# Kernel tuning notes

Measured on AMD Instinct MI355X. Metric: run time of the kernel, lower is better.

## Reference

```python
import jax, jax.numpy as jnp
import numpy as np

B, N, IN_DIM, EMB, HEADS, M, ITERS = 8, 4096, 1024, 512, 4, 256, 6
DH = EMB // HEADS
SCALE = DH ** -0.5
RES_K = 33  # residual depthwise conv kernel size (TransMIL / nystrom-attention default)


def setup_inputs() -> dict:
    key = jax.random.key(0)
    ks = iter(jax.random.split(key, 40))
    def rn(shape, s=0.02):
        return jax.random.normal(next(ks), shape, jnp.float32) * s
    inp = {"X": jax.random.normal(next(ks), (B, N, IN_DIM), jnp.float32)}
    inp["few_w"] = rn((IN_DIM, EMB)); inp["few_b"] = jnp.zeros((EMB,), jnp.float32)
    inp["cls_token"] = rn((1, 1, EMB), 1.0)
    for i in (1, 2):
        inp[f"l{i}_ln_g"] = jnp.ones((EMB,), jnp.float32)
        inp[f"l{i}_ln_b"] = jnp.zeros((EMB,), jnp.float32)
        inp[f"l{i}_qkv_w"] = rn((EMB, 3 * EMB))
        inp[f"l{i}_out_w"] = rn((EMB, EMB))
        inp[f"l{i}_out_b"] = jnp.zeros((EMB,), jnp.float32)
        inp[f"l{i}_res_k"] = rn((HEADS, 1, RES_K, 1))
    for ksz in (7, 5, 3):
        inp[f"ppeg_k{ksz}"] = rn((EMB, 1, ksz, ksz))
        inp[f"ppeg_b{ksz}"] = jnp.zeros((EMB,), jnp.float32)
    inp["norm_g"] = jnp.ones((EMB,), jnp.float32)
    inp["norm_b"] = jnp.zeros((EMB,), jnp.float32)
    inp["cls_w"] = rn((EMB, 1)); inp["cls_b"] = jnp.zeros((1,), jnp.float32)
    return inp


def _ln(x, g, b):
    mu = x.mean(-1, keepdims=True)
    var = x.var(-1, keepdims=True)
    return (x - mu) / jnp.sqrt(var + 1e-5) * g + b


def _pinv(x, iters):
    # Moore-Penrose iterative pseudo-inverse of (..., m, m)
    abs_x = jnp.abs(x)
    z = jnp.swapaxes(x, -1, -2) / (abs_x.sum(-1).max() * abs_x.sum(-2).max())
    I = jnp.eye(x.shape[-1], dtype=x.dtype)
    for _ in range(iters):
        xz = x @ z
        z = 0.25 * z @ (13 * I - xz @ (15 * I - xz @ (7 * I - xz)))
    return z


def _nystrom_layer(x, ln_g, ln_b, qkv_w, out_w, out_b, res_k):
    # pre-norm transformer layer with Nystrom attention + residual depthwise conv
    b, n, d = x.shape
    h = _ln(x, ln_g, ln_b)
    pad = (-n) % M  # left-pad so seq divisible by n_landmarks
    hp = jnp.pad(h, ((0, 0), (pad, 0), (0, 0)))
    n_p = n + pad
    q, k, v = jnp.split(hp @ qkv_w, 3, axis=-1)
    def to_heads(t):
        return t.reshape(b, n_p, HEADS, DH).transpose(0, 2, 1, 3)  # (b,h,n,dh)
    q, k, v = to_heads(q) * SCALE, to_heads(k), to_heads(v)
    l = n_p // M
    q_l = q.reshape(b, HEADS, M, l, DH).mean(3)  # landmark means
    k_l = k.reshape(b, HEADS, M, l, DH).mean(3)
    a1 = jax.nn.softmax(jnp.einsum('bhid,bhjd->bhij', q, k_l), -1)    # (b,h,n,m)
    a2 = jax.nn.softmax(jnp.einsum('bhid,bhjd->bhij', q_l, k_l), -1)  # (b,h,m,m)
    a3 = jax.nn.softmax(jnp.einsum('bhid,bhjd->bhij', q_l, k), -1)    # (b,h,m,n)
    out = a1 @ (_pinv(a2, ITERS) @ (a3 @ v))
    # residual depthwise conv over sequence, one channel per head
    res = jax.lax.conv_general_dilated(
        v, res_k, (1, 1), ((RES_K // 2, RES_K // 2), (0, 0)),
        dimension_numbers=('NCHW', 'OIHW', 'NCHW'), feature_group_count=HEADS)
    out = out + res
    out = out.transpose(0, 2, 1, 3).reshape(b, n_p, d) @ out_w + out_b
    return x + out[:, -n:]


def _dwconv(x, k, bias, pad):
    y = jax.lax.conv_general_dilated(
        x, k, (1, 1), ((pad, pad), (pad, pad)),
        dimension_numbers=('NCHW', 'OIHW', 'NCHW'), feature_group_count=EMB)
    return y + bias[None, :, None, None]


def _ppeg(x, H, W, k7, b7, k5, b5, k3, b3):
    b, _, c = x.shape
    cls_t, feat = x[:, :1], x[:, 1:]
    f = feat.transpose(0, 2, 1).reshape(b, c, H, W)
    y = f + _dwconv(f, k7, b7, 3) + _dwconv(f, k5, b5, 2) + _dwconv(f, k3, b3, 1)
    y = y.reshape(b, c, H * W).transpose(0, 2, 1)
    return jnp.concatenate([cls_t, y], axis=1)


def _forward(X, few_w, few_b, cls_token,
             l1_ln_g, l1_ln_b, l1_qkv_w, l1_out_w, l1_out_b, l1_res_k,
             l2_ln_g, l2_ln_b, l2_qkv_w, l2_out_w, l2_out_b, l2_res_k,
             ppeg_k7, ppeg_b7, ppeg_k5, ppeg_b5, ppeg_k3, ppeg_b3,
             norm_g, norm_b, cls_w, cls_b):
    b, bag = X.shape[0], X.shape[1]
    h = X @ few_w + few_b
    ps = int(np.ceil(np.sqrt(bag)))
    add = ps * ps - bag
    h = jnp.concatenate([h, h[:, :add]], axis=1)  # pad bag to perfect square
    h = jnp.concatenate([jnp.broadcast_to(cls_token, (b, 1, EMB)), h], axis=1)
    h = _nystrom_layer(h, l1_ln_g, l1_ln_b, l1_qkv_w, l1_out_w, l1_out_b, l1_res_k)
    h = _ppeg(h, ps, ps, ppeg_k7, ppeg_b7, ppeg_k5, ppeg_b5, ppeg_k3, ppeg_b3)
    h = _nystrom_layer(h, l2_ln_g, l2_ln_b, l2_qkv_w, l2_out_w, l2_out_b, l2_res_k)
    h = _ln(h, norm_g, norm_b)
    return (h[:, 0] @ cls_w + cls_b).squeeze(-1)  # (batch,) bag logits


def reference(X, few_w, few_b, cls_token,
              l1_ln_g, l1_ln_b, l1_qkv_w, l1_out_w, l1_out_b, l1_res_k,
              l2_ln_g, l2_ln_b, l2_qkv_w, l2_out_w, l2_out_b, l2_res_k,
              ppeg_k7, ppeg_b7, ppeg_k5, ppeg_b5, ppeg_k3, ppeg_b3,
              norm_g, norm_b, cls_w, cls_b):
    return _forward(X, few_w, few_b, cls_token,
                    l1_ln_g, l1_ln_b, l1_qkv_w, l1_out_w, l1_out_b, l1_res_k,
                    l2_ln_g, l2_ln_b, l2_qkv_w, l2_out_w, l2_out_b, l2_res_k,
                    ppeg_k7, ppeg_b7, ppeg_k5, ppeg_b5, ppeg_k3, ppeg_b3,
                    norm_g, norm_b, cls_w, cls_b)
```

## Files before the change

### kernel.cpp

```cpp
#include <hip/hip_runtime.h>

constexpr int BATCH = 8;
constexpr int NTOK  = 4097;
constexpr int NP    = 4352;
constexpr int PADR  = 255;
constexpr int EMBD  = 512;
constexpr int DHD   = 128;
constexpr int LSUB  = 17;
constexpr float SCALE_F = 0.08838834764831845f;

constexpr int PPS   = 72;
constexpr int PPLN  = 72 * 70;
constexpr long long TPAD_FLOATS = (long long)BATCH * EMBD * PPLN;

typedef unsigned short u16;
typedef short   s16x8 __attribute__((ext_vector_type(8)));
typedef u16     u16x4 __attribute__((ext_vector_type(4)));
typedef float   f32x4 __attribute__((ext_vector_type(4)));

__device__ __forceinline__ u16 f2bf(float x) {
    unsigned u = __float_as_uint(x);
    u += 0x7fffu + ((u >> 16) & 1u);
    return (u16)(u >> 16);
}
__device__ __forceinline__ float bf2f(u16 h) {
    return __uint_as_float(((unsigned)h) << 16);
}

__device__ __forceinline__ float block_sum256(float v) {
    __shared__ float tmp[4];
    __syncthreads();
#pragma unroll
    for (int off = 32; off > 0; off >>= 1) v += __shfl_down(v, off, 64);
    int t = threadIdx.x;
    if ((t & 63) == 0) tmp[t >> 6] = v;
    __syncthreads();
    return tmp[0] + tmp[1] + tmp[2] + tmp[3];
}

__device__ __forceinline__ float block_max256(float v) {
    __shared__ float tmp[4];
    __syncthreads();
#pragma unroll
    for (int off = 32; off > 0; off >>= 1) v = fmaxf(v, __shfl_down(v, off, 64));
    int t = threadIdx.x;
    if ((t & 63) == 0) tmp[t >> 6] = v;
    __syncthreads();
    return fmaxf(fmaxf(tmp[0], tmp[1]), fmaxf(tmp[2], tmp[3]));
}

struct GemmP {
    const float* A; const float* B; float* C; const float* bias;
    long long As1, As2, Bs1, Bs2, Cs1, Cs2;
    int Adiv, Bdiv, Cdiv;
    int Am, Bk, Bn, Cm, Arow, Crow;
    int M, N, K, nb;
    float alpha; int accum;
    float bdiagc; int btrans; float cdiagc; int ctrans;
};

constexpr int LDSTR = 40;
constexpr int AH = 0, AL = 2560, BHs = 5120, BLs = 7680;

__global__ __launch_bounds__(256) void gemm_k(GemmP p) {
    __shared__ u16 lds[10240];
    const int bz = blockIdx.z;
    const float* Ab = p.A + (long long)(bz / p.Adiv) * p.As1 + (long long)(bz % p.Adiv) * p.As2;
    const float* Bb = p.B + (long long)(bz / p.Bdiv) * p.Bs1 + (long long)(bz % p.Bdiv) * p.Bs2;
    float*       Cb = p.C + (long long)(bz / p.Cdiv) * p.Cs1 + (long long)(bz % p.Cdiv) * p.Cs2;
    const int m0 = blockIdx.y * 64, n0 = blockIdx.x * 64;
    const int t = threadIdx.x;
    const int wave = t >> 6, lane = t & 63;
    const int wm = (wave & 1) * 32, wn = (wave >> 1) * 32;
    const int quad = lane >> 4, l15 = lane & 15;

    f32x4 acc[2][2];
#pragma unroll
    for (int i = 0; i < 2; ++i)
#pragma unroll
        for (int j = 0; j < 2; ++j) acc[i][j] = (f32x4){0.f, 0.f, 0.f, 0.f};

    for (int k0 = 0; k0 < p.K; k0 += 32) {
        {
            const int ar = t >> 2, ac = (t & 3) * 8;
            float v[8];
            if (m0 + ar < p.M) {
                const float* s = Ab + (long long)(m0 + ar + p.Arow) * p.Am + (k0 + ac);
                float4 x0 = *(const float4*)s, x1 = *(const float4*)(s + 4);
                v[0] = x0.x; v[1] = x0.y; v[2] = x0.z; v[3] = x0.w;
                v[4] = x1.x; v[5] = x1.y; v[6] = x1.z; v[7] = x1.w;
            } else {
#pragma unroll
                for (int i = 0; i < 8; ++i) v[i] = 0.f;
            }
            u16 h[8], l[8];
#pragma unroll
            for (int i = 0; i < 8; ++i) { h[i] = f2bf(v[i]); l[i] = f2bf(v[i] - bf2f(h[i])); }
            const int off = ar * LDSTR + ac;
            u16x4 a0, a1, b0, b1;
#pragma unroll
            for (int i = 0; i < 4; ++i) { a0[i] = h[i]; a1[i] = h[i + 4]; b0[i] = l[i]; b1[i] = l[i + 4]; }
            *(u16x4*)&lds[AH + off] = a0; *(u16x4*)&lds[AH + off + 4] = a1;
            *(u16x4*)&lds[AL + off] = b0; *(u16x4*)&lds[AL + off + 4] = b1;
        }
        if (p.Bn == 1) {
            const int bk = t >> 3, n8 = (t & 7) * 8;
            const float* s = Bb + (long long)(k0 + bk) * p.Bk + (n0 + n8);
            float4 x0 = *(const float4*)s, x1 = *(const float4*)(s + 4);
            float v[8] = {x0.x, x0.y, x0.z, x0.w, x1.x, x1.y, x1.z, x1.w};
            if (p.btrans) {
                const int gk = k0 + bk;
#pragma unroll
                for (int i = 0; i < 8; ++i)
                    v[i] = (gk == n0 + n8 + i ? p.bdiagc : 0.f) - v[i];
            }
#pragma unroll
            for (int i = 0; i < 8; ++i) {
                int j = (i + (t & 7)) & 7;
                u16 h = f2bf(v[j]);
                lds[BHs + (n8 + j) * LDSTR + bk] = h;
                lds[BLs + (n8 + j) * LDSTR + bk] = f2bf(v[j] - bf2f(h));
            }
        } else {
            const int bn = t >> 2, k8 = (t & 3) * 8;
            const float* s = Bb + (long long)(n0 + bn) * p.Bn + (k0 + k8);
            float4 x0 = *(const float4*)s, x1 = *(const float4*)(s + 4);
            float v[8] = {x0.x, x0.y, x0.z, x0.w, x1.x, x1.y, x1.z, x1.w};
            u16 h[8], l[8];
#pragma unroll
            for (int i = 0; i < 8; ++i) { h[i] = f2bf(v[i]); l[i] = f2bf(v[i] - bf2f(h[i])); }
            const int off = bn * LDSTR + k8;
            u16x4 a0, a1, b0, b1;
#pragma unroll
            for (int i = 0; i < 4; ++i) { a0[i] = h[i]; a1[i] = h[i + 4]; b0[i] = l[i]; b1[i] = l[i + 4]; }
            *(u16x4*)&lds[BHs + off] = a0; *(u16x4*)&lds[BHs + off + 4] = a1;
            *(u16x4*)&lds[BLs + off] = b0; *(u16x4*)&lds[BLs + off + 4] = b1;
        }
        __syncthreads();

        s16x8 ah[2], al[2], bh[2], bl[2];
#pragma unroll
        for (int mi = 0; mi < 2; ++mi) {
            const int off = (wm + mi * 16 + l15) * LDSTR + quad * 8;
            u16x4 q0 = *(const u16x4*)&lds[AH + off], q1 = *(const u16x4*)&lds[AH + off + 4];
            u16x4 r0 = *(const u16x4*)&lds[AL + off], r1 = *(const u16x4*)&lds[AL + off + 4];
            s16x8 fh, fl;
#pragma unroll
            for (int i = 0; i < 4; ++i) { fh[i] = q0[i]; fh[i + 4] = q1[i]; fl[i] = r0[i]; fl[i + 4] = r1[i]; }
            ah[mi] = fh; al[mi] = fl;
        }
#pragma unroll
        for (int ni = 0; ni < 2; ++ni) {
            const int off = (wn + ni * 16 + l15) * LDSTR + quad * 8;
            u16x4 q0 = *(const u16x4*)&lds[BHs + off], q1 = *(const u16x4*)&lds[BHs + off + 4];
            u16x4 r0 = *(const u16x4*)&lds[BLs + off], r1 = *(const u16x4*)&lds[BLs + off + 4];
            s16x8 fh, fl;
#pragma unroll
            for (int i = 0; i < 4; ++i) { fh[i] = q0[i]; fh[i + 4] = q1[i]; fl[i] = r0[i]; fl[i + 4] = r1[i]; }
            bh[ni] = fh; bl[ni] = fl;
        }
#pragma unroll
        for (int mi = 0; mi < 2; ++mi)
#pragma unroll
            for (int ni = 0; ni < 2; ++ni) {
                acc[mi][ni] = __builtin_amdgcn_mfma_f32_16x16x32_bf16(ah[mi], bh[ni], acc[mi][ni], 0, 0, 0);
                acc[mi][ni] = __builtin_amdgcn_mfma_f32_16x16x32_bf16(ah[mi], bl[ni], acc[mi][ni], 0, 0, 0);
                acc[mi][ni] = __builtin_amdgcn_mfma_f32_16x16x32_bf16(al[mi], bh[ni], acc[mi][ni], 0, 0, 0);
            }
        __syncthreads();
    }

#pragma unroll
    for (int mi = 0; mi < 2; ++mi)
#pragma unroll
        for (int ni = 0; ni < 2; ++ni) {
            const int n = n0 + wn + ni * 16 + l15;
#pragma unroll
            for (int r = 0; r < 4; ++r) {
                const int m = m0 + wm + mi * 16 + quad * 4 + r;
                if (m >= p.M) continue;
                float v = p.alpha * acc[mi][ni][r];
                if (p.bias) v += p.bias[n];
                if (p.ctrans) v = (m == n ? p.cdiagc : 0.f) - v;
                float* dst = Cb + (long long)(m + p.Crow) * p.Cm + n;
                if (p.accum) *dst += v; else *dst = v;
            }
        }
}

struct SplitP {
    const float* src; u16* dh; u16* dl;
    long long s1, s2, rstride, dstride, total;
    int div, R, C8;
    float scale;
};
__global__ __launch_bounds__(256) void split_k(SplitP p) {
    long long idx = (long long)blockIdx.x * 256 + threadIdx.x;
    if (idx >= p.total) return;
    int c8 = (int)(idx % p.C8);
    long long tmp = idx / p.C8;
    int r  = (int)(tmp % p.R);
    int bz = (int)(tmp / p.R);
    const float* s = p.src + (long long)(bz / p.div) * p.s1 + (long long)(bz % p.div) * p.s2
                   + (long long)r * p.rstride + c8 * 8;
    float4 x0 = *(const float4*)s, x1 = *(const float4*)(s + 4);
    float v[8] = {x0.x, x0.y, x0.z, x0.w, x1.x, x1.y, x1.z, x1.w};
    s16x8 hv, lv;
#pragma unroll
    for (int i = 0; i < 8; ++i) {
        float sv = v[i] * p.scale;
        u16 h = f2bf(sv);
        hv[i] = (short)h;
        lv[i] = (short)f2bf(sv - bf2f(h));
    }
    long long doff = (long long)bz * p.dstride + (long long)r * (p.C8 * 8) + c8 * 8;
    *(s16x8*)&p.dh[doff] = hv;
    *(s16x8*)&p.dl[doff] = lv;
}

__global__ __launch_bounds__(256) void splitT_k(const float* __restrict__ src,
                                                u16* __restrict__ dh, u16* __restrict__ dl,
                                                int K, int N) {
    int idx = blockIdx.x * 256 + threadIdx.x;
    if (idx >= N * K) return;
    int n = idx / K, k = idx - n * K;
    float v = src[(long long)k * N + n];
    u16 h = f2bf(v);
    dh[idx] = h;
    dl[idx] = f2bf(v - bf2f(h));
}

struct GemmBtP {
    const u16 *Ah, *Al, *Bh, *Bl;
    float* C; const float* bias;
    long long Abs, Bbs, Cbs;
    int M, N, K, Cm, Crow, accum;
};

__global__ __launch_bounds__(512, 4) void gemm_bt_k(GemmBtP p) {
    __shared__ u16 lds[10240];
    const int bz = blockIdx.z;
    const u16* Ahb = p.Ah + (long long)bz * p.Abs;
    const u16* Alb = p.Al + (long long)bz * p.Abs;
    const u16* Bhb = p.Bh + (long long)bz * p.Bbs;
    const u16* Blb = p.Bl + (long long)bz * p.Bbs;
    float*     Cb  = p.C  + (long long)bz * p.Cbs;
    const int m0 = blockIdx.y * 128, n0 = blockIdx.x * 256;
    const int t = threadIdx.x;
    const int wave = t >> 6, lane = t & 63;
    const int wm = (wave & 1) * 64, wn = (wave >> 1) * 64;
    const int quad = lane >> 4, l15 = lane & 15;
    const int K = p.K;

    const int r0 = t >> 2, c0 = (t & 3) * 8;
    const int ga0 = (m0 + r0 < p.M) ? (m0 + r0) : (p.M - 1);
    const long long arow0 = (long long)ga0 * K + c0;
    const long long bb0   = (long long)(n0 + wn + l15) * K + quad * 8;
    const long long bstep = 16LL * K;
    const int wof = r0 * LDSTR + c0;

    f32x4 acc[4][4];
#pragma unroll
    for (int i = 0; i < 4; ++i)
#pragma unroll
        for (int j = 0; j < 4; ++j) acc[i][j] = (f32x4){0.f, 0.f, 0.f, 0.f};

    s16x8 sa0, sl0;
    auto LOADA = [&](int k0) {
        sa0 = *(const s16x8*)&Ahb[arow0 + k0];
        sl0 = *(const s16x8*)&Alb[arow0 + k0];
    };
    LOADA(0);

    for (int k0 = 0; k0 < K; k0 += 32) {
        *(s16x8*)&lds[wof]        = sa0;
        *(s16x8*)&lds[5120 + wof] = sl0;
        __syncthreads();
        if (k0 + 32 < K) LOADA(k0 + 32);

        s16x8 bh[4], bl[4];
#pragma unroll
        for (int ni = 0; ni < 4; ++ni) {
            const long long bo = bb0 + ni * bstep + k0;
            bh[ni] = *(const s16x8*)&Bhb[bo];
            bl[ni] = *(const s16x8*)&Blb[bo];
        }
#pragma unroll
        for (int mi = 0; mi < 4; ++mi) {
            const int off = (wm + mi * 16 + l15) * LDSTR + quad * 8;
            s16x8 ah = *(const s16x8*)&lds[off];
            s16x8 al = *(const s16x8*)&lds[5120 + off];
#pragma unroll
            for (int ni = 0; ni < 4; ++ni) {
                acc[mi][ni] = __builtin_amdgcn_mfma_f32_16x16x32_bf16(ah, bh[ni], acc[mi][ni], 0, 0, 0);
                acc[mi][ni] = __builtin_amdgcn_mfma_f32_16x16x32_bf16(ah, bl[ni], acc[mi][ni], 0, 0, 0);
                acc[mi][ni] = __builtin_amdgcn_mfma_f32_16x16x32_bf16(al, bh[ni], acc[mi][ni], 0, 0, 0);
            }
        }
        __syncthreads();
    }

#pragma unroll
    for (int mi = 0; mi < 4; ++mi)
#pragma unroll
        for (int ni = 0; ni < 4; ++ni) {
            const int n = n0 + wn + ni * 16 + l15;
            const float bv = p.bias ? p.bias[n] : 0.f;
#pragma unroll
            for (int r = 0; r < 4; ++r) {
                const int m = m0 + wm + mi * 16 + quad * 4 + r;
                if (m >= p.M) continue;
                float* dst = Cb + (long long)(m + p.Crow) * p.Cm + n;
                float v = acc[mi][ni][r] + bv;
                if (p.accum) *dst += v; else *dst = v;
            }
        }
}

__global__ void cls_set_k(float* H0, const float* cls) {
    int t = blockIdx.x * 256 + threadIdx.x;
    int b = t >> 9, c = t & 511;
    H0[(long long)b * NTOK * EMBD + c] = cls[c];
}

__global__ __launch_bounds__(256) void ln_pad_k(const float* __restrict__ H0,
                                                u16* __restrict__ oh, u16* __restrict__ ol,
                                                const float* g, const float* bb) {
    int row = blockIdx.x, b = blockIdx.y, t = threadIdx.x;
    long long off = ((long long)b * NP + row) * EMBD;
    if (row < PADR) {
        oh[off + t] = 0; oh[off + t + 256] = 0;
        ol[off + t] = 0; ol[off + t + 256] = 0;
        return;
    }
    const float* x = H0 + ((long long)b * NTOK + (row - PADR)) * EMBD;
    float v0 = x[t], v1 = x[t + 256];
    float mu = block_sum256(v0 + v1) * (1.f / EMBD);
    float d0 = v0 - mu, d1 = v1 - mu;
    float var = block_sum256(d0 * d0 + d1 * d1) * (1.f / EMBD);
    float rs = 1.f / sqrtf(var + 1e-5f);
    float y0 = d0 * rs * g[t]       + bb[t];
    float y1 = d1 * rs * g[t + 256] + bb[t + 256];
    u16 h0 = f2bf(y0); oh[off + t]       = h0; ol[off + t]       = f2bf(y0 - bf2f(h0));
    u16 h1 = f2bf(y1); oh[off + t + 256] = h1; ol[off + t + 256] = f2bf(y1 - bf2f(h1));
}

__global__ void landmark_k(const float* __restrict__ QKV, float* __restrict__ QL,
                           float* __restrict__ KL) {
    long long idx = (long long)blockIdx.x * 256 + threadIdx.x;
    int d = idx & 127; int i = (int)((idx >> 7) & 255); int bh = (int)(idx >> 15);
    int b = bh >> 2, h = bh & 3;
    const float* base = QKV + (long long)b * NP * 1536 + (long long)i * LSUB * 1536 + h * DHD + d;
    float sq = 0.f, sk = 0.f;
#pragma unroll
    for (int j = 0; j < LSUB; ++j) { sq += base[j * 1536]; sk += base[j * 1536 + EMBD]; }
    QL[idx] = sq * (1.f / LSUB);
    KL[idx] = sk * (1.f / LSUB);
}

__global__ __launch_bounds__(256) void softmax256_k(float* __restrict__ X) {
    long long row = (long long)blockIdx.x * 4 + (threadIdx.x >> 6);
    int lane = threadIdx.x & 63;
    float4* p = (float4*)(X + row * 256) + lane;
    float4 v = *p;
    float m = fmaxf(fmaxf(v.x, v.y), fmaxf(v.z, v.w));
#pragma unroll
    for (int off = 32; off > 0; off >>= 1) m = fmaxf(m, __shfl_xor(m, off, 64));
    float ex = __expf(v.x - m), ey = __expf(v.y - m), ez = __expf(v.z - m), ew = __expf(v.w - m);
    float s = ex + ey + ez + ew;
#pragma unroll
    for (int off = 32; off > 0; off >>= 1) s += __shfl_xor(s, off, 64);
    float inv = 1.f / s;
    *p = make_float4(ex * inv, ey * inv, ez * inv, ew * inv);
}

__global__ __launch_bounds__(256) void softmax_k(float* __restrict__ X, int L) {
    float4* p = (float4*)(X + (long long)blockIdx.x * L);
    int nv = L >> 2, t = threadIdx.x;
    float m = -1e30f;
    for (int i = t; i < nv; i += 256) {
        float4 v = p[i];
        m = fmaxf(m, fmaxf(fmaxf(v.x, v.y), fmaxf(v.z, v.w)));
    }
    m = block_max256(m);
    float s = 0.f;
    for (int i = t; i < nv; i += 256) {
        float4 v = p[i];
        v.x = __expf(v.x - m); v.y = __expf(v.y - m); v.z = __expf(v.z - m); v.w = __expf(v.w - m);
        p[i] = v;
        s += v.x + v.y + v.z + v.w;
    }
    s = block_sum256(s);
    float inv = 1.f / s;
    for (int i = t; i < nv; i += 256) {
        float4 v = p[i];
        p[i] = make_float4(v.x * inv, v.y * inv, v.z * inv, v.w * inv);
    }
}

__global__ __launch_bounds__(256) void pinv_absmax_k(const float* __restrict__ X, float* red) {
    int bh = blockIdx.x, t = threadIdx.x;
    const float* x = X + (long long)bh * 65536;
    float rs = 0.f, cs = 0.f;
    for (int j = 0; j < 256; ++j) { rs += fabsf(x[t * 256 + j]); cs += fabsf(x[j * 256 + t]); }
    float mr = block_max256(rs);
    float mc = block_max256(cs);
    if (t == 0) { red[bh] = mr; red[32 + bh] = mc; }
}

__global__ void pinv_scalar_k(const float* red, float* inv) {
    float mr = 0.f, mc = 0.f;
    for (int i = 0; i < 32; ++i) { mr = fmaxf(mr, red[i]); mc = fmaxf(mc, red[32 + i]); }
    inv[0] = 1.f / (mr * mc);
}

__global__ void pinv_tinit_k(const float* __restrict__ X, const float* __restrict__ inv,
                             float* __restrict__ Z) {
    long long idx = (long long)blockIdx.x * 256 + threadIdx.x;
    int j = (int)(idx & 255); int i = (int)((idx >> 8) & 255); long long bh = idx >> 16;
    Z[idx] = X[(bh << 16) + ((long long)j << 8) + i] * inv[0];
}

__global__ void resconv_k(const float* __restrict__ QKV, const float* __restrict__ rk,
                          float* __restrict__ ATT2) {
    long long idx = (long long)blockIdx.x * 256 + threadIdx.x;
    if (idx >= (long long)BATCH * NTOK * EMBD) return;
    int c = (int)(idx & 511); long long r = idx >> 9;
    int n = PADR + (int)(r % NTOK); int b = (int)(r / NTOK);
    int h = c >> 7, d = c & 127;
    const float* vb = QKV + (long long)b * NP * 1536 + 1024 + h * DHD + d;
    float acc = 0.f;
#pragma unroll
    for (int u = 0; u < 33; ++u) {
        int nn = n + u - 16;
        if (nn >= 0 && nn < NP) acc += vb[(long long)nn * 1536] * rk[h * 33 + u];
    }
    ATT2[((long long)b * NP + n) * EMBD + c] += acc;
}

__global__ void wsum_k(const float* __restrict__ k7, const float* __restrict__ k5,
                       const float* __restrict__ k3, const float* __restrict__ b7,
                       const float* __restrict__ b5, const float* __restrict__ b3,
                       float* __restrict__ W) {
    int idx = blockIdx.x * 256 + threadIdx.x;
    if (idx < 25088) {
        int c = idx / 49, i = idx - c * 49;
        int dy = i / 7, dx = i - dy * 7;
        float w = k7[idx];
        if (dy >= 1 && dy <= 5 && dx >= 1 && dx <= 5) w += k5[c * 25 + (dy - 1) * 5 + (dx - 1)];
        if (dy >= 2 && dy <= 4 && dx >= 2 && dx <= 4) w += k3[c * 9 + (dy - 2) * 3 + (dx - 2)];
        W[idx] = w;
    } else if (idx < 25600) {
        int c = idx - 25088;
        W[25088 + c] = b7[c] + b5[c] + b3[c];
    }
}

__global__ __launch_bounds__(256) void tin_k(const float* __restrict__ H0,
                                             float* __restrict__ Tpad) {
    __shared__ float lds[64][65];
    const int y = blockIdx.x, c0 = blockIdx.y * 64, b = blockIdx.z;
    const int t = threadIdx.x;
    const int pc = t & 63, pr4 = t >> 6;
    const float* src = H0 + ((long long)b * NTOK + 1 + y * 64) * EMBD + c0;
#pragma unroll
    for (int i = 0; i < 16; ++i) {
        int pr = pr4 + i * 4;
        lds[pr][pc] = src[(long long)pr * EMBD + pc];
    }
    __syncthreads();
    const int xw = t & 63, cw4 = t >> 6;
#pragma unroll
    for (int i = 0; i < 16; ++i) {
        int cw = cw4 + i * 4;
        Tpad[(long long)(b * 512 + c0 + cw) * PPLN + (3 + y) * PPS + 3 + xw] = lds[xw][cw];
    }
}

__global__ __launch_bounds__(256, 4) void conv7_k(const float* __restrict__ Tpad,
                                                  const float* __restrict__ Wall,
                                                  float* __restrict__ Tout) {
    const int bc = blockIdx.x;
    const int c = bc & 511;
    const int t = threadIdx.x;
    const int x = t & 63, band = t >> 6;
    const int y0 = band * 16;
    const float* in = Tpad + (long long)bc * PPLN + x;
    float* outp = Tout + (long long)bc * 4096 + x;

    float W[49];
#pragma unroll
    for (int i = 0; i < 49; ++i) W[i] = Wall[c * 49 + i];
    const float bias = Wall[25088 + c];

    float win[7][7];
#pragma unroll
    for (int j = 0; j < 6; ++j)
#pragma unroll
        for (int d = 0; d < 7; ++d)
            win[j][d] = in[(y0 + j) * PPS + d];

#pragma unroll
    for (int yy = 0; yy < 16; ++yy) {
        const int slot = (6 + yy) % 7;
#pragma unroll
        for (int d = 0; d < 7; ++d)
            win[slot][d] = in[(y0 + yy + 6) * PPS + d];
        float s = bias + win[(yy + 3) % 7][3];
#pragma unroll
        for (int dy = 0; dy < 7; ++dy) {
            const int r = (yy + dy) % 7;
#pragma unroll
            for (int dx = 0; dx < 7; ++dx)
                s += W[dy * 7 + dx] * win[r][dx];
        }
        outp[(y0 + yy) * 64] = s;
    }
}

__global__ __launch_bounds__(256) void tout_k(const float* __restrict__ Tout,
                                              float* __restrict__ H0) {
    __shared__ float lds[64][65];
    const int y = blockIdx.x, c0 = blockIdx.y * 64, b = blockIdx.z;
    const int t = threadIdx.x;
    const int xl = t & 63, cl4 = t >> 6;
#pragma unroll
    for (int i = 0; i < 16; ++i) {
        int cl = cl4 + i * 4;
        lds[xl][cl] = Tout[(long long)(b * 512 + c0 + cl) * 4096 + y * 64 + xl];
    }
    __syncthreads();
    const int pc = t & 63, pl4 = t >> 6;
    float* dst = H0 + ((long long)b * NTOK + 1 + y * 64) * EMBD + c0;
#pragma unroll
    for (int i = 0; i < 16; ++i) {
        int pl = pl4 + i * 4;
        dst[(long long)pl * EMBD + pc] = lds[pl][pc];
    }
}

__global__ __launch_bounds__(256) void head_k(const float* __restrict__ H0, const float* g,
                                              const float* bb, const float* cw, const float* cb,
                                              float* __restrict__ out) {
    int b = blockIdx.x, t = threadIdx.x;
    const float* x = H0 + (long long)b * NTOK * EMBD;
    float v0 = x[t], v1 = x[t + 256];
    float mu = block_sum256(v0 + v1) * (1.f / EMBD);
    float d0 = v0 - mu, d1 = v1 - mu;
    float var = block_sum256(d0 * d0 + d1 * d1) * (1.f / EMBD);
    float rs = 1.f / sqrtf(var + 1e-5f);
    float y0 = d0 * rs * g[t] + bb[t];
    float y1 = d1 * rs * g[t + 256] + bb[t + 256];
    float s = block_sum256(y0 * cw[t] + y1 * cw[t + 256]);
    if (t == 0) out[b] = s + cb[0];
}

extern "C" void kernel_launch(void* const* d_in, const int* in_sizes, int n_in,
                              void* d_out, int out_size, void* d_ws, size_t ws_size,
                              hipStream_t stream) {
    (void)in_sizes; (void)n_in; (void)out_size; (void)ws_size;
    const float* X        = (const float*)d_in[0];
    const float* few_w    = (const float*)d_in[1];
    const float* few_b    = (const float*)d_in[2];
    const float* cls_tok  = (const float*)d_in[3];
    const float* ln_g[2]  = {(const float*)d_in[4],  (const float*)d_in[10]};
    const float* ln_b[2]  = {(const float*)d_in[5],  (const float*)d_in[11]};
    const float* qkv_w[2] = {(const float*)d_in[6],  (const float*)d_in[12]};
    const float* out_w[2] = {(const float*)d_in[7],  (const float*)d_in[13]};
    const float* out_b[2] = {(const float*)d_in[8],  (const float*)d_in[14]};
    const float* res_k[2] = {(const float*)d_in[9],  (const float*)d_in[15]};
    const float* k7 = (const float*)d_in[16]; const float* b7 = (const float*)d_in[17];
    const float* k5 = (const float*)d_in[18]; const float* b5 = (const float*)d_in[19];
    const float* k3 = (const float*)d_in[20]; const float* b3 = (const float*)d_in[21];
    const float* norm_g = (const float*)d_in[22]; const float* norm_b = (const float*)d_in[23];
    const float* cls_w  = (const float*)d_in[24]; const float* cls_b  = (const float*)d_in[25];
    float* out = (float*)d_out;

    float* ws  = (float*)d_ws;
    float* H0  = ws;
    float* LNH = H0  + 16781312LL;
    float* QKV = LNH + 17825792LL;
    float* A3  = QKV + 53477376LL;
    float* QL  = A3  + 35651584LL;
    float* KL  = QL  + 1048576LL;
    float* A2  = KL  + 1048576LL;
    float* KV  = A2  + 2097152LL;
    float* ZKV = KV  + 1048576LL;
    float* RED = ZKV + 1048576LL;

    u16* LNHh = (u16*)LNH;
    u16* LNHl = (u16*)(LNH + 8912896LL);
    u16* QLh  = (u16*)KV;
    u16* QLl  = (u16*)(KV + 524288LL);
    u16* KLh  = (u16*)ZKV;
    u16* KLl  = (u16*)(ZKV + 524288LL);
    u16* Xh   = (u16*)A3;
    u16* Xl   = (u16*)(A3 + 16777216LL);
    u16* ATh  = (u16*)A3;
    u16* ATl  = (u16*)(A3 + 8390656LL);
    u16* Wh   = (u16*)A2;
    u16* fwl  = (u16*)(A2 + 262144LL);
    u16* qwl  = (u16*)(A2 + 393216LL);
    u16* owl  = (u16*)(A2 + 131072LL);
    float* Zb0 = LNH;
    float* Zb1 = LNH + 2097152LL;
    float* XZm = LNH + 4194304LL;
    float* U1  = LNH + 6291456LL;
    float* U2  = LNH + 8388608LL;
    float* Tpad = QKV;
    float* Tout = QKV + TPAD_FLOATS;
    float* WSUM = A3;

    auto gemmx = [&](const float* A, long long As1, long long As2, int Adiv, int Am, int Arow,
                     const float* Bm, long long Bs1, long long Bs2, int Bdiv, int Bk, int Bn,
                     float* C, long long Cs1, long long Cs2, int Cdiv, int Cm, int Crow,
                     int M, int N, int K, int nb, float alpha, int accum, const float* bias,
                     float bdiagc, int btrans, float cdiagc, int ctrans) {
        GemmP p;
        p.A = A; p.B = Bm; p.C = C; p.bias = bias;
        p.As1 = As1; p.As2 = As2; p.Bs1 = Bs1; p.Bs2 = Bs2; p.Cs1 = Cs1; p.Cs2 = Cs2;
        p.Adiv = Adiv; p.Bdiv = Bdiv; p.Cdiv = Cdiv;
        p.Am = Am; p.Bk = Bk; p.Bn = Bn; p.Cm = Cm; p.Arow = Arow; p.Crow = Crow;
        p.M = M; p.N = N; p.K = K; p.nb = nb; p.alpha = alpha; p.accum = accum;
        p.bdiagc = bdiagc; p.btrans = btrans; p.cdiagc = cdiagc; p.ctrans = ctrans;
        dim3 grid(N / 64, (M + 63) / 64, nb);
        gemm_k<<<grid, 256, 0, stream>>>(p);
    };
    auto gemm = [&](const float* A, long long As1, long long As2, int Adiv, int Am, int Arow,
                    const float* Bm, long long Bs1, long long Bs2, int Bdiv, int Bk, int Bn,
                    float* C, long long Cs1, long long Cs2, int Cdiv, int Cm, int Crow,
                    int M, int N, int K, int nb, float alpha, int accum, const float* bias) {
        gemmx(A, As1, As2, Adiv, Am, Arow, Bm, Bs1, Bs2, Bdiv, Bk, Bn,
              C, Cs1, Cs2, Cdiv, Cm, Crow, M, N, K, nb, alpha, accum, bias, 0.f, 0, 0.f, 0);
    };
    auto split = [&](const float* src, u16* dh, u16* dl, long long s1, long long s2, int div,
                     long long rstride, int R, int C, int nb, float scale) {
        SplitP p;
        p.src = src; p.dh = dh; p.dl = dl;
        p.s1 = s1; p.s2 = s2; p.div = div;
        p.rstride = rstride; p.R = R; p.C8 = C >> 3;
        p.dstride = (long long)R * C;
        p.total = (long long)nb * R * (C >> 3);
        p.scale = scale;
        int blocks = (int)((p.total + 255) / 256);
        split_k<<<blocks, 256, 0, stream>>>(p);
    };
    auto gemmbt = [&](const u16* Ah, const u16* Al, long long Abs,
                      const u16* Bh, const u16* Bl, long long Bbs,
                      float* C, long long Cbs, int Cm, int Crow,
                      int M, int N, int K, int nb, int accum, const float* bias) {
        GemmBtP p;
        p.Ah = Ah; p.Al = Al; p.Bh = Bh; p.Bl = Bl;
        p.C = C; p.bias = bias;
        p.Abs = Abs; p.Bbs = Bbs; p.Cbs = Cbs;
        p.M = M; p.N = N; p.K = K; p.Cm = Cm; p.Crow = Crow; p.accum = accum;
        dim3 grid(N / 256, (M + 127) / 128, nb);
        gemm_bt_k<<<grid, 512, 0, stream>>>(p);
    };

    cls_set_k<<<16, 256, 0, stream>>>(H0, cls_tok);
    split(X, Xh, Xl, 0, 0, 1, 1024, 32768, 1024, 1, 1.f);
    splitT_k<<<2048, 256, 0, stream>>>(few_w, Wh, fwl, 1024, 512);
    gemmbt(Xh, Xl, 4194304LL, Wh, fwl, 0,
           H0, 2097664LL, 512, 1,
           4096, 512, 1024, BATCH, 0, few_b);

    for (int L = 0; L < 2; ++L) {
        ln_pad_k<<<dim3(NP, BATCH), 256, 0, stream>>>(H0, LNHh, LNHl, ln_g[L], ln_b[L]);
        splitT_k<<<3072, 256, 0, stream>>>(qkv_w[L], Wh, qwl, 512, 1536);
        gemmbt(LNHh, LNHl, 0, Wh, qwl, 0,
               QKV, 0, 1536, 0,
               34816, 1536, 512, 1, 0, nullptr);
        landmark_k<<<4096, 256, 0, stream>>>(QKV, QL, KL);
        gemm(QL, 32768LL, 0, 1, 128, 0,
             KL, 32768LL, 0, 1, 1, 128,
             A2, 65536LL, 0, 1, 256, 0,
             256, 256, 128, 32, SCALE_F, 0, nullptr);
        softmax256_k<<<2048, 256, 0, stream>>>(A2);
        split(QL, QLh, QLl, 32768LL, 0, 1, 128, 256, 128, 32, SCALE_F);
        split(KL, KLh, KLl, 32768LL, 0, 1, 128, 256, 128, 32, 1.f);
        split(QKV + 512, LNHh, LNHl, 6680064LL, 128LL, 4, 1536, 4352, 128, 32, 1.f);
        gemmbt(QLh, QLl, 32768LL, LNHh, LNHl, 557056LL,
               A3, 1114112LL, 4352, 0,
               256, 4352, 128, 32, 0, nullptr);
        softmax_k<<<8192, 256, 0, stream>>>(A3, 4352);
        gemm(A3, 1114112LL, 0, 1, 4352, 0,
             QKV + 1024, 6680064LL, 128LL, 4, 1536, 1,
             KV, 32768LL, 0, 1, 128, 0,
             256, 128, 4352, 32, 1.f, 0, nullptr);
        split(QKV, LNHh, LNHl, 6680064LL, 128LL, 4, 1536, 4352, 128, 32, SCALE_F);
        gemmbt(LNHh, LNHl, 557056LL, KLh, KLl, 32768LL,
               A3, 1114112LL, 256, 0,
               4352, 256, 128, 32, 0, nullptr);
        softmax256_k<<<34816, 256, 0, stream>>>(A3);
        pinv_absmax_k<<<32, 256, 0, stream>>>(A2, RED);
        pinv_scalar_k<<<1, 1, 0, stream>>>(RED, RED + 64);
        pinv_tinit_k<<<8192, 256, 0, stream>>>(A2, RED + 64, Zb0);
        float* zc = Zb0; float* zn = Zb1;
        for (int it = 0; it < 6; ++it) {
            gemm(A2, 65536LL, 0, 1, 256, 0, zc, 65536LL, 0, 1, 256, 1,
                 XZm, 65536LL, 0, 1, 256, 0, 256, 256, 256, 32, 1.f, 0, nullptr);
            gemmx(XZm, 65536LL, 0, 1, 256, 0, XZm, 65536LL, 0, 1, 256, 1,
                  U1, 65536LL, 0, 1, 256, 0, 256, 256, 256, 32, 1.f, 0, nullptr,
                  7.f, 1, 15.f, 1);
            gemmx(XZm, 65536LL, 0, 1, 256, 0, U1, 65536LL, 0, 1, 256, 1,
                  U2, 65536LL, 0, 1, 256, 0, 256, 256, 256, 32, 1.f, 0, nullptr,
                  0.f, 0, 13.f, 1);
            gemm(zc, 65536LL, 0, 1, 256, 0, U2, 65536LL, 0, 1, 256, 1,
                 zn, 65536LL, 0, 1, 256, 0, 256, 256, 256, 32, 0.25f, 0, nullptr);
            float* t2 = zc; zc = zn; zn = t2;
        }
        gemm(zc, 65536LL, 0, 1, 256, 0,
             KV, 32768LL, 0, 1, 128, 1,
             ZKV, 32768LL, 0, 1, 128, 0,
             256, 128, 256, 32, 1.f, 0, nullptr);
        gemm(A3, 1114112LL, 0, 1, 256, 0,
             ZKV, 32768LL, 0, 1, 128, 1,
             LNH, 2228224LL, 128LL, 4, 512, 0,
             4352, 128, 256, 32, 1.f, 0, nullptr);
        resconv_k<<<65552, 256, 0, stream>>>(QKV, res_k[L], LNH);
        split(LNH + PADR * 512, ATh, ATl, 2228224LL, 0, 1, 512, 4097, 512, 8, 1.f);
        splitT_k<<<1024, 256, 0, stream>>>(out_w[L], Wh, owl, 512, 512);
        gemmbt(ATh, ATl, 2097664LL, Wh, owl, 0,
               H0, 2097664LL, 512, 0,
               4097, 512, 512, BATCH, 1, out_b[L]);

        if (L == 0) {
            hipMemsetAsync(Tpad, 0, TPAD_FLOATS * sizeof(float), stream);
            wsum_k<<<101, 256, 0, stream>>>(k7, k5, k3, b7, b5, b3, WSUM);
            tin_k<<<dim3(64, 8, 8), 256, 0, stream>>>(H0, Tpad);
            conv7_k<<<4096, 256, 0, stream>>>(Tpad, WSUM, Tout);
            tout_k<<<dim3(64, 8, 8), 256, 0, stream>>>(Tout, H0);
        }
    }

    head_k<<<BATCH, 256, 0, stream>>>(H0, norm_g, norm_b, cls_w, cls_b, out);
}
```

Measured before the change: 4.634 ms.

## Double-buffer GEMM A tiles via direct global-to-LDS loads and XCD-aware block remap

The A-operand staging in the split-bf16 GEMM now uses global_load_lds to write directly into a double-buffered LDS tile. This removes the register round-trip and one barrier per K step, and lets the next tile's load overlap the current MFMA work. Block IDs are also remapped so consecutive tiles land on the same XCD, which should improve L2 reuse. The costs are a larger LDS footprint (32KB, which may lower occupancy) and an unpadded 32-element row stride that may cause LDS bank conflicts.

```diff
diff --git a/kernel.cpp b/kernel.cpp
--- a/kernel.cpp
+++ b/kernel.cpp
@@ -25,6 +25,13 @@
 }
 __device__ __forceinline__ float bf2f(u16 h) {
     return __uint_as_float(((unsigned)h) << 16);
+}
+
+__device__ __forceinline__ void gload16(const u16* gp, u16* lp) {
+    __builtin_amdgcn_global_load_lds(
+        (const __attribute__((address_space(1))) unsigned int*)gp,
+        (__attribute__((address_space(3))) unsigned int*)lp,
+        16, 0, 0);
 }
 
 __device__ __forceinline__ float block_sum256(float v) {
@@ -238,26 +245,36 @@
 };
 
 __global__ __launch_bounds__(512, 4) void gemm_bt_k(GemmBtP p) {
-    __shared__ u16 lds[10240];
+    __shared__ __align__(16) u16 lds[16384];
     const int bz = blockIdx.z;
     const u16* Ahb = p.Ah + (long long)bz * p.Abs;
     const u16* Alb = p.Al + (long long)bz * p.Abs;
     const u16* Bhb = p.Bh + (long long)bz * p.Bbs;
     const u16* Blb = p.Bl + (long long)bz * p.Bbs;
     float*     Cb  = p.C  + (long long)bz * p.Cbs;
-    const int m0 = blockIdx.y * 128, n0 = blockIdx.x * 256;
+
+    const int NX = gridDim.x;
+    const int nwg = NX * gridDim.y;
+    const int bid = blockIdx.y * NX + blockIdx.x;
+    const int qq = nwg >> 3, rr = nwg & 7;
+    const int xcd = bid & 7, loc = bid >> 3;
+    const int nbid = (xcd < rr) ? (xcd * (qq + 1) + loc)
+                                : (rr * (qq + 1) + (xcd - rr) * qq + loc);
+    const int m0 = (nbid / NX) * 128, n0 = (nbid % NX) * 256;
+
     const int t = threadIdx.x;
     const int wave = t >> 6, lane = t & 63;
     const int wm = (wave & 1) * 64, wn = (wave >> 1) * 64;
     const int quad = lane >> 4, l15 = lane & 15;
     const int K = p.K;
 
-    const int r0 = t >> 2, c0 = (t & 3) * 8;
-    const int ga0 = (m0 + r0 < p.M) ? (m0 + r0) : (p.M - 1);
-    const long long arow0 = (long long)ga0 * K + c0;
+    const int srow = 16 * wave + (lane >> 2);
+    const int sga  = (m0 + srow < p.M) ? (m0 + srow) : (p.M - 1);
+    const long long sbase = (long long)sga * K + (lane & 3) * 8;
+    u16* ldsw = &lds[wave * 512];
+
     const long long bb0   = (long long)(n0 + wn + l15) * K + quad * 8;
     const long long bstep = 16LL * K;
-    const int wof = r0 * LDSTR + c0;
 
     f32x4 acc[4][4];
 #pragma unroll
@@ -265,19 +282,14 @@
 #pragma unroll
         for (int j = 0; j < 4; ++j) acc[i][j] = (f32x4){0.f, 0.f, 0.f, 0.f};
 
-    s16x8 sa0, sl0;
-    auto LOADA = [&](int k0) {
-        sa0 = *(const s16x8*)&Ahb[arow0 + k0];
-        sl0 = *(const s16x8*)&Alb[arow0 + k0];
-    };
-    LOADA(0);
-
-    for (int k0 = 0; k0 < K; k0 += 32) {
-        *(s16x8*)&lds[wof]        = sa0;
-        *(s16x8*)&lds[5120 + wof] = sl0;
-        __syncthreads();
-        if (k0 + 32 < K) LOADA(k0 + 32);
-
+    gload16(Ahb + sbase, ldsw);
+    gload16(Alb + sbase, ldsw + 4096);
+    __syncthreads();
+
+    const int nt = K >> 5;
+    int cur = 0;
+    for (int t0 = 0; t0 < nt; ++t0) {
+        const int k0 = t0 << 5;
         s16x8 bh[4], bl[4];
 #pragma unroll
         for (int ni = 0; ni < 4; ++ni) {
@@ -285,11 +297,17 @@
             bh[ni] = *(const s16x8*)&Bhb[bo];
             bl[ni] = *(const s16x8*)&Blb[bo];
         }
+        if (t0 + 1 < nt) {
+            u16* dst = ldsw + (cur ^ 1) * 8192;
+            gload16(Ahb + sbase + k0 + 32, dst);
+            gload16(Alb + sbase + k0 + 32, dst + 4096);
+        }
+        const int bufo = cur * 8192;
 #pragma unroll
         for (int mi = 0; mi < 4; ++mi) {
-            const int off = (wm + mi * 16 + l15) * LDSTR + quad * 8;
+            const int off = bufo + (wm + mi * 16 + l15) * 32 + quad * 8;
             s16x8 ah = *(const s16x8*)&lds[off];
-            s16x8 al = *(const s16x8*)&lds[5120 + off];
+            s16x8 al = *(const s16x8*)&lds[off + 4096];
 #pragma unroll
             for (int ni = 0; ni < 4; ++ni) {
                 acc[mi][ni] = __builtin_amdgcn_mfma_f32_16x16x32_bf16(ah, bh[ni], acc[mi][ni], 0, 0, 0);
@@ -298,6 +316,7 @@
             }
         }
         __syncthreads();
+        cur ^= 1;
     }
 
 #pragma unroll
```

New measurement: 4.372 ms. -5.7%, faster.
